# Kernel tuning notes

Measured on AMD Instinct MI355X. Metric: run time of the kernel, lower is better.

The kernel has to match this reference:

```python
import jax, jax.numpy as jnp
import numpy as np

D_MODEL = 1024
NUM_HEADS = 16
D_K = D_MODEL // NUM_HEADS


def setup_inputs() -> dict:
    key = jax.random.key(0)
    ks = jax.random.split(key, 12)
    B, L, D = 1, 4096, D_MODEL
    s = 1.0 / np.sqrt(D)
    return {
        "q": jax.random.normal(ks[0], (B, L, D), jnp.float32),
        "k": jax.random.normal(ks[1], (B, L, D), jnp.float32),
        "v": jax.random.normal(ks[2], (B, L, D), jnp.float32),
        "wq": jax.random.normal(ks[3], (D, D), jnp.float32) * s,
        "bq": jnp.zeros((D,), jnp.float32),
        "wk": jax.random.normal(ks[4], (D, D), jnp.float32) * s,
        "bk": jnp.zeros((D,), jnp.float32),
        "wv": jax.random.normal(ks[5], (D, D), jnp.float32) * s,
        "bv": jnp.zeros((D,), jnp.float32),
        "wo": jax.random.normal(ks[6], (D, D), jnp.float32) * s,
        "bo": jnp.zeros((D,), jnp.float32),
    }


def reference(q, k, v, wq, bq, wk, bk, wv, bv, wo, bo):
    B, L, D = q.shape
    H, dk = NUM_HEADS, D_K
    # linear projections then split heads: [B, L, D] -> [B, H, L, dk]
    def proj(x, w, b):
        return (x @ w.T + b).reshape(B, L, H, dk).transpose(0, 2, 1, 3)
    qh = proj(q, wq, bq)
    kh = proj(k, wk, bk)
    vh = proj(v, wv, bv)
    scores = jnp.einsum("bhqd,bhkd->bhqk", qh, kh) / jnp.sqrt(jnp.float32(dk))
    attn = jax.nn.softmax(scores, axis=-1)  # [B, H, L, L]
    out = jnp.einsum("bhqk,bhkd->bhqd", attn, vh)
    out = out.transpose(0, 2, 1, 3).reshape(B, L, D)
    return out @ wo.T + bo
```

## Files before the change

### kernel.cpp

```cpp
#include <hip/hip_runtime.h>
#include <hip/hip_bf16.h>
#include <stdint.h>


typedef __bf16 bf16_t;
typedef __bf16 bf16x8 __attribute__((ext_vector_type(8)));
typedef __bf16 bf16x4 __attribute__((ext_vector_type(4)));
typedef float f32x4 __attribute__((ext_vector_type(4)));
typedef unsigned short u16x8 __attribute__((ext_vector_type(8)));

#define MFMA_BF16 __builtin_amdgcn_mfma_f32_16x16x32_bf16

__device__ __forceinline__ void async_copy16(const void* g, void* lds) {
  __builtin_amdgcn_global_load_lds(
      (__attribute__((address_space(1))) void*)(uintptr_t)g,
      (__attribute__((address_space(3))) void*)lds, 16, 0, 0);
}

__global__ __launch_bounds__(256) void cast_f32_bf16(
    const float* __restrict__ s0, bf16_t* __restrict__ d0, int n0,
    const float* __restrict__ s1, bf16_t* __restrict__ d1, int n1,
    const float* __restrict__ s2, bf16_t* __restrict__ d2, int n2,
    const float* __restrict__ s3, bf16_t* __restrict__ d3, int n3,
    const float* __restrict__ s4, bf16_t* __restrict__ d4, int n4,
    const float* __restrict__ s5, bf16_t* __restrict__ d5, int n5,
    const float* __restrict__ s6, bf16_t* __restrict__ d6, int n6) {
  const float* s;
  bf16_t* d;
  int n;
  switch (blockIdx.z) {
    case 0: s = s0; d = d0; n = n0; break;
    case 1: s = s1; d = d1; n = n1; break;
    case 2: s = s2; d = d2; n = n2; break;
    case 3: s = s3; d = d3; n = n3; break;
    case 4: s = s4; d = d4; n = n4; break;
    case 5: s = s5; d = d5; n = n5; break;
    default: s = s6; d = d6; n = n6; break;
  }
  const int i = (blockIdx.x * 256 + threadIdx.x) * 8;
  if (i >= n) return;
  float4 a = *(const float4*)(s + i);
  float4 b = *(const float4*)(s + i + 4);
  bf16x8 o;
  o[0] = (bf16_t)a.x; o[1] = (bf16_t)a.y; o[2] = (bf16_t)a.z; o[3] = (bf16_t)a.w;
  o[4] = (bf16_t)b.x; o[5] = (bf16_t)b.y; o[6] = (bf16_t)b.z; o[7] = (bf16_t)b.w;
  *(bf16x8*)(d + i) = o;
}

template <typename CT>
__global__ __launch_bounds__(256) void gemm3_bt(
    const bf16_t* __restrict__ A0, const bf16_t* __restrict__ W0,
    const float* __restrict__ b0, CT* __restrict__ C0,
    const bf16_t* __restrict__ A1, const bf16_t* __restrict__ W1,
    const float* __restrict__ b1, CT* __restrict__ C1,
    const bf16_t* __restrict__ A2, const bf16_t* __restrict__ W2,
    const float* __restrict__ b2, CT* __restrict__ C2,
    int M, int N, int K) {
  const bf16_t *A, *W;
  const float* bias;
  CT* C;
  if (blockIdx.z == 0)      { A = A0; W = W0; bias = b0; C = C0; }
  else if (blockIdx.z == 1) { A = A1; W = W1; bias = b1; C = C1; }
  else                      { A = A2; W = W2; bias = b2; C = C2; }

  __shared__ bf16_t As[128][32];
  __shared__ bf16_t Bs[128][32];

  const int t = threadIdx.x;
  const int w = t >> 6, lane = t & 63;
  const int quad = lane >> 4, l16 = lane & 15;
  const int wr = w >> 1, wc = w & 1;
  const int m0 = blockIdx.x * 128;
  const int n0 = blockIdx.y * 128;
  const int srow = lane >> 2;
  const int scol = (lane & 3) * 8;

  f32x4 acc[4][4] = {};

  for (int k0 = 0; k0 < K; k0 += 32) {
    async_copy16(&A[(size_t)(m0 + (2 * w) * 16 + srow) * K + k0 + scol],
                 (char*)As + (2 * w) * 1024);
    async_copy16(&A[(size_t)(m0 + (2 * w + 1) * 16 + srow) * K + k0 + scol],
                 (char*)As + (2 * w + 1) * 1024);
    async_copy16(&W[(size_t)(n0 + (2 * w) * 16 + srow) * K + k0 + scol],
                 (char*)Bs + (2 * w) * 1024);
    async_copy16(&W[(size_t)(n0 + (2 * w + 1) * 16 + srow) * K + k0 + scol],
                 (char*)Bs + (2 * w + 1) * 1024);
    __syncthreads();

    bf16x8 af[4], bfr[4];
#pragma unroll
    for (int mt = 0; mt < 4; mt++)
      af[mt] = *(const bf16x8*)&As[wr * 64 + mt * 16 + l16][quad * 8];
#pragma unroll
    for (int nt = 0; nt < 4; nt++)
      bfr[nt] = *(const bf16x8*)&Bs[wc * 64 + nt * 16 + l16][quad * 8];
#pragma unroll
    for (int mt = 0; mt < 4; mt++)
#pragma unroll
      for (int nt = 0; nt < 4; nt++)
        acc[mt][nt] = MFMA_BF16(af[mt], bfr[nt], acc[mt][nt], 0, 0, 0);
    __syncthreads();
  }

#pragma unroll
  for (int nt = 0; nt < 4; nt++) {
    const int col = n0 + wc * 64 + nt * 16 + l16;
    const float bb = bias[col];
#pragma unroll
    for (int mt = 0; mt < 4; mt++) {
#pragma unroll
      for (int r = 0; r < 4; r++) {
        const int row = m0 + wr * 64 + mt * 16 + quad * 4 + r;
        C[(size_t)row * N + col] = (CT)(acc[mt][nt][r] + bb);
      }
    }
  }
}

__global__ __launch_bounds__(256) void frag_tile(
    const bf16_t* __restrict__ s0, bf16_t* __restrict__ d0,
    const bf16_t* __restrict__ s1, bf16_t* __restrict__ d1,
    const bf16_t* __restrict__ s2, bf16_t* __restrict__ d2) {
  const bf16_t* src;
  bf16_t* dst;
  const int z = blockIdx.z;
  if (z == 0)      { src = s0; dst = d0; }
  else if (z == 1) { src = s1; dst = d1; }
  else             { src = s2; dst = d2; }

  const int h = blockIdx.y;
  const int l0 = blockIdx.x * 64;
  const int t = threadIdx.x;

  __shared__ ushort Ts[64][72];

#pragma unroll
  for (int p = 0; p < 2; p++) {
    const int r = p * 32 + (t >> 3);
    const int c = (t & 7) * 8;
    float4 v = *(const float4*)(src + (size_t)(l0 + r) * 1024 + h * 64 + c);
    *(float4*)&Ts[r][c] = v;
  }
  __syncthreads();

  if (z < 2) {
    const float qscale = 0.125f * 1.44269504088896340736f;
#pragma unroll
    for (int p = 0; p < 2; p++) {
      const int gi = p * 256 + t;
      const int l16 = gi & 15, quad = (gi >> 4) & 3, kc = (gi >> 6) & 1;
      const int tl = gi >> 7;
      float4 v = *(const float4*)&Ts[tl * 16 + l16][kc * 32 + quad * 8];
      if (z == 0) {
        bf16x8 b = *(bf16x8*)&v;
#pragma unroll
        for (int e = 0; e < 8; e++) b[e] = (bf16_t)((float)b[e] * qscale);
        v = *(float4*)&b;
      }
      *(float4*)(dst + (size_t)(h * 256 + (l0 >> 4) + tl) * 1024 +
                 (size_t)(kc * 64 + quad * 16 + l16) * 8) = v;
    }
  } else {
#pragma unroll
    for (int p = 0; p < 2; p++) {
      const int gi = p * 256 + t;
      const int l16 = gi & 15, quad = (gi >> 4) & 3, kvc = (gi >> 6) & 1;
      const int dkt = gi >> 7;
      u16x8 tmp;
#pragma unroll
      for (int e = 0; e < 8; e++)
        tmp[e] = Ts[kvc * 32 + quad * 4 + (e & 3) + 16 * (e >> 2)]
                   [dkt * 16 + l16];
      *(u16x8*)(dst + (size_t)(h * 256 + (l0 >> 6) * 4 + dkt) * 1024 +
                (size_t)(kvc * 64 + quad * 16 + l16) * 8) = tmp;
    }
  }
}

__global__ __launch_bounds__(512, 4) void flash_attn(
    const bf16_t* __restrict__ Qt, const bf16_t* __restrict__ Kt,
    const bf16_t* __restrict__ Vt, bf16_t* __restrict__ O, int L) {
  const int i = blockIdx.x;
  const int slot = i >> 3;
  const int h = (i & 7) * 2 + (slot >> 5);
  const int qblk = slot & 31;

  const int t = threadIdx.x;
  const int w = t >> 6, lane = t & 63;
  const int quad = lane >> 4, l16 = lane & 15;
  const int g = w >> 2;
  const int ws = w & 3;
  const int tq0 = qblk * 8 + ws * 2;

  __shared__ bf16_t Kst[2][8192];
  __shared__ bf16_t Vst[2][8192];

  const size_t hb = (size_t)h * 256 * 1024;

  union V8 {
    bf16x8 v8;
    bf16x4 v4[2];
  };

  bf16x8 qa[2][2];
#pragma unroll
  for (int qt = 0; qt < 2; qt++)
#pragma unroll
    for (int kc = 0; kc < 2; kc++)
      qa[qt][kc] = *(const bf16x8*)(Qt + hb + (size_t)(tq0 + qt) * 1024 +
                                    kc * 512 + lane * 8);

#define STAGE(mc_, buf_)                                                      \
  {                                                                           \
    const size_t pb_ = hb + (size_t)(mc_) * 8192;                             \
    async_copy16(Kt + pb_ + (size_t)t * 8, (char*)&Kst[buf_][0] + w * 1024);  \
    async_copy16(Kt + pb_ + 4096 + (size_t)t * 8,                             \
                 (char*)&Kst[buf_][0] + 8192 + w * 1024);                     \
    async_copy16(Vt + pb_ + (size_t)t * 8, (char*)&Vst[buf_][0] + w * 1024);  \
    async_copy16(Vt + pb_ + 4096 + (size_t)t * 8,                             \
                 (char*)&Vst[buf_][0] + 8192 + w * 1024);                     \
  }

  STAGE(0, 0);

  f32x4 oT[2][4] = {};
  float ls[2] = {0.f, 0.f};

  const int laneK = lane * 16;

  const int NMC = L / 128;
  for (int mc = 0; mc < NMC; mc++) {
    const int buf = mc & 1;
    __syncthreads();
    if (mc + 1 < NMC) STAGE(mc + 1, buf ^ 1);

    const char* Kc = (const char*)&Kst[buf][0] + g * 8192;
    const char* Vc = (const char*)&Vst[buf][0] + g * 8192;

    f32x4 sT[2][4];
#pragma unroll
    for (int tt = 0; tt < 4; tt++) {
      const bf16x8 k0 = *(const bf16x8*)(Kc + tt * 2048 + laneK);
      const bf16x8 k1 = *(const bf16x8*)(Kc + tt * 2048 + 1024 + laneK);
#pragma unroll
      for (int qt = 0; qt < 2; qt++) {
        f32x4 z = {0.f, 0.f, 0.f, 0.f};
        z = MFMA_BF16(k0, qa[qt][0], z, 0, 0, 0);
        z = MFMA_BF16(k1, qa[qt][1], z, 0, 0, 0);
        sT[qt][tt] = z;
      }
    }

    V8 pb[2][2];
#pragma unroll
    for (int qt = 0; qt < 2; qt++) {
#pragma unroll
      for (int tt = 0; tt < 4; tt++) {
        bf16x4 pk;
        float rs = 0.f;
#pragma unroll
        for (int r = 0; r < 4; r++) {
          const float pv = __builtin_amdgcn_exp2f(sT[qt][tt][r]);
          rs += pv;
          pk[r] = (bf16_t)pv;
        }
        ls[qt] += rs;
        pb[qt][tt >> 1].v4[tt & 1] = pk;
      }
    }

#pragma unroll
    for (int dkt = 0; dkt < 4; dkt++) {
#pragma unroll
      for (int kvc = 0; kvc < 2; kvc++) {
        const bf16x8 vv =
            *(const bf16x8*)(Vc + dkt * 2048 + kvc * 1024 + laneK);
#pragma unroll
        for (int qt = 0; qt < 2; qt++)
          oT[qt][dkt] = MFMA_BF16(vv, pb[qt][kvc].v8, oT[qt][dkt], 0, 0, 0);
      }
    }
  }
#undef STAGE

  __syncthreads();
  float* sc0 = (float*)&Kst[0][0];
  float* sc1 = (float*)&Vst[0][0];
  const int sidx = (ws * 64 + lane) * 20;
  if (g == 1) {
#pragma unroll
    for (int dkt = 0; dkt < 4; dkt++) {
      *(f32x4*)(sc0 + sidx + dkt * 4) = oT[0][dkt];
      *(f32x4*)(sc1 + sidx + dkt * 4) = oT[1][dkt];
    }
    sc0[sidx + 16] = ls[0];
    sc1[sidx + 16] = ls[1];
  }
  __syncthreads();
  if (g == 0) {
#pragma unroll
    for (int dkt = 0; dkt < 4; dkt++) {
      oT[0][dkt] += *(const f32x4*)(sc0 + sidx + dkt * 4);
      oT[1][dkt] += *(const f32x4*)(sc1 + sidx + dkt * 4);
    }
    ls[0] += sc0[sidx + 16];
    ls[1] += sc1[sidx + 16];

#pragma unroll
    for (int qt = 0; qt < 2; qt++) {
      float l = ls[qt];
      l += __shfl_xor(l, 16);
      l += __shfl_xor(l, 32);
      const float inv = 1.0f / l;
      const size_t row = (size_t)(tq0 + qt) * 16 + l16;
#pragma unroll
      for (int dkt = 0; dkt < 4; dkt++)
#pragma unroll
        for (int r = 0; r < 4; r++)
          O[row * 1024 + h * 64 + dkt * 16 + quad * 4 + r] =
              (bf16_t)(oT[qt][dkt][r] * inv);
    }
  }
}

extern "C" void kernel_launch(void* const* d_in, const int* in_sizes, int n_in,
                              void* d_out, int out_size, void* d_ws,
                              size_t ws_size, hipStream_t stream) {
  const float* q  = (const float*)d_in[0];
  const float* k  = (const float*)d_in[1];
  const float* v  = (const float*)d_in[2];
  const float* wq = (const float*)d_in[3];
  const float* bq = (const float*)d_in[4];
  const float* wk = (const float*)d_in[5];
  const float* bk = (const float*)d_in[6];
  const float* wv = (const float*)d_in[7];
  const float* bv = (const float*)d_in[8];
  const float* wo = (const float*)d_in[9];
  const float* bo = (const float*)d_in[10];
  float* out = (float*)d_out;

  const int L = 4096, D = 1024;
  const int nLD = L * D;
  const int nDD = D * D;
  bf16_t* p = (bf16_t*)d_ws;
  bf16_t* qb  = p; p += nLD;
  bf16_t* kb  = p; p += nLD;
  bf16_t* vb  = p; p += nLD;
  bf16_t* wqb = p; p += nDD;
  bf16_t* wkb = p; p += nDD;
  bf16_t* wvb = p; p += nDD;
  bf16_t* wob = p; p += nDD;
  bf16_t* Qp  = p; p += nLD;
  bf16_t* Kp  = p; p += nLD;
  bf16_t* Vp  = p; p += nLD;
  bf16_t* Qt  = p; p += nLD;
  bf16_t* Kt  = p; p += nLD;
  bf16_t* Vt  = p; p += nLD;
  bf16_t* Op  = Qp;

  dim3 blk(256);
  cast_f32_bf16<<<dim3(nLD / (256 * 8), 1, 7), blk, 0, stream>>>(
      q, qb, nLD, k, kb, nLD, v, vb, nLD, wq, wqb, nDD, wk, wkb, nDD,
      wv, wvb, nDD, wo, wob, nDD);
  gemm3_bt<bf16_t><<<dim3(L / 128, D / 128, 3), blk, 0, stream>>>(
      qb, wqb, bq, Qp, kb, wkb, bk, Kp, vb, wvb, bv, Vp, L, D, D);
  frag_tile<<<dim3(L / 64, 16, 3), blk, 0, stream>>>(Qp, Qt, Kp, Kt, Vp, Vt);
  flash_attn<<<dim3((L / 128) * 16), dim3(512), 0, stream>>>(Qt, Kt, Vt, Op, L);
  gemm3_bt<float><<<dim3(L / 128, D / 128, 1), blk, 0, stream>>>(
      Op, wob, bo, out, Op, wob, bo, out, Op, wob, bo, out, L, D, D);
}
```

Before: 264.0 us.

## Fuse fragment retiling into QKV GEMM epilogue and split attention loop barriers

The QKV projection GEMM now writes its outputs directly in the MFMA fragment layout that flash attention consumes, with the Q scale folded in. This removes the separate frag_tile kernel and its extra global read/write pass. The attention loop is also restructured into two phases, QK+softmax and PV, with explicit vmcnt waits, barriers and s_setprio around the MFMA sections, so K and V staging can overlap compute. The cost is scattered, narrow global stores in the GEMM epilogue and more fragile hand-coded wait counts.

```diff
diff --git a/kernel.cpp b/kernel.cpp
--- a/kernel.cpp
+++ b/kernel.cpp
@@ -47,21 +47,21 @@
   *(bf16x8*)(d + i) = o;
 }
 
-template <typename CT>
-__global__ __launch_bounds__(256) void gemm3_bt(
+__global__ __launch_bounds__(256) void gemm_qkv(
     const bf16_t* __restrict__ A0, const bf16_t* __restrict__ W0,
-    const float* __restrict__ b0, CT* __restrict__ C0,
+    const float* __restrict__ b0, bf16_t* __restrict__ D0,
     const bf16_t* __restrict__ A1, const bf16_t* __restrict__ W1,
-    const float* __restrict__ b1, CT* __restrict__ C1,
+    const float* __restrict__ b1, bf16_t* __restrict__ D1,
     const bf16_t* __restrict__ A2, const bf16_t* __restrict__ W2,
-    const float* __restrict__ b2, CT* __restrict__ C2,
+    const float* __restrict__ b2, bf16_t* __restrict__ D2,
     int M, int N, int K) {
   const bf16_t *A, *W;
   const float* bias;
-  CT* C;
-  if (blockIdx.z == 0)      { A = A0; W = W0; bias = b0; C = C0; }
-  else if (blockIdx.z == 1) { A = A1; W = W1; bias = b1; C = C1; }
-  else                      { A = A2; W = W2; bias = b2; C = C2; }
+  bf16_t* D;
+  const int zz = blockIdx.z;
+  if (zz == 0)      { A = A0; W = W0; bias = b0; D = D0; }
+  else if (zz == 1) { A = A1; W = W1; bias = b1; D = D1; }
+  else              { A = A2; W = W2; bias = b2; D = D2; }
 
   __shared__ bf16_t As[128][32];
   __shared__ bf16_t Bs[128][32];
@@ -103,6 +103,95 @@
     __syncthreads();
   }
 
+  if (zz < 2) {
+    const float qs = (zz == 0) ? 0.125f * 1.44269504088896340736f : 1.0f;
+#pragma unroll
+    for (int nt = 0; nt < 4; nt++) {
+      const int col = n0 + wc * 64 + nt * 16 + l16;
+      const int hh = col >> 6, dk = col & 63;
+      const float bb = bias[col];
+      const size_t cbase =
+          (size_t)hh * 256 * 1024 +
+          (size_t)((dk >> 5) * 64 + ((dk >> 3) & 3) * 16) * 8 + (dk & 7);
+#pragma unroll
+      for (int mt = 0; mt < 4; mt++) {
+        const int rowtile = (m0 >> 4) + wr * 4 + mt;
+#pragma unroll
+        for (int r = 0; r < 4; r++) {
+          const int rl = quad * 4 + r;
+          D[cbase + (size_t)rowtile * 1024 + rl * 8] =
+              (bf16_t)((acc[mt][nt][r] + bb) * qs);
+        }
+      }
+    }
+  } else {
+#pragma unroll
+    for (int nt = 0; nt < 4; nt++) {
+      const int col = n0 + wc * 64 + nt * 16 + l16;
+      const int hh = col >> 6, dk = col & 63;
+      const float bb = bias[col];
+#pragma unroll
+      for (int mt = 0; mt < 4; mt++) {
+        const int kvb = m0 + wr * 64 + mt * 16 + quad * 4;
+        const int r50 = kvb & 31;
+        bf16x4 pk;
+#pragma unroll
+        for (int r = 0; r < 4; r++) pk[r] = (bf16_t)(acc[mt][nt][r] + bb);
+        const size_t addr =
+            (size_t)(hh * 256 + (kvb >> 6) * 4 + (dk >> 4)) * 1024 +
+            (size_t)(((kvb >> 5) & 1) * 64 + ((r50 & 15) >> 2) * 16 +
+                     (dk & 15)) * 8 +
+            (((r50 >> 4) & 1) << 2);
+        *(bf16x4*)(D + addr) = pk;
+      }
+    }
+  }
+}
+
+__global__ __launch_bounds__(256) void gemm_out(
+    const bf16_t* __restrict__ A, const bf16_t* __restrict__ W,
+    const float* __restrict__ bias, float* __restrict__ C, int M, int N,
+    int K) {
+  __shared__ bf16_t As[128][32];
+  __shared__ bf16_t Bs[128][32];
+
+  const int t = threadIdx.x;
+  const int w = t >> 6, lane = t & 63;
+  const int quad = lane >> 4, l16 = lane & 15;
+  const int wr = w >> 1, wc = w & 1;
+  const int m0 = blockIdx.x * 128;
+  const int n0 = blockIdx.y * 128;
+  const int srow = lane >> 2;
+  const int scol = (lane & 3) * 8;
+
+  f32x4 acc[4][4] = {};
+
+  for (int k0 = 0; k0 < K; k0 += 32) {
+    async_copy16(&A[(size_t)(m0 + (2 * w) * 16 + srow) * K + k0 + scol],
+                 (char*)As + (2 * w) * 1024);
+    async_copy16(&A[(size_t)(m0 + (2 * w + 1) * 16 + srow) * K + k0 + scol],
+                 (char*)As + (2 * w + 1) * 1024);
+    async_copy16(&W[(size_t)(n0 + (2 * w) * 16 + srow) * K + k0 + scol],
+                 (char*)Bs + (2 * w) * 1024);
+    async_copy16(&W[(size_t)(n0 + (2 * w + 1) * 16 + srow) * K + k0 + scol],
+                 (char*)Bs + (2 * w + 1) * 1024);
+    __syncthreads();
+
+    bf16x8 af[4], bfr[4];
+#pragma unroll
+    for (int mt = 0; mt < 4; mt++)
+      af[mt] = *(const bf16x8*)&As[wr * 64 + mt * 16 + l16][quad * 8];
+#pragma unroll
+    for (int nt = 0; nt < 4; nt++)
+      bfr[nt] = *(const bf16x8*)&Bs[wc * 64 + nt * 16 + l16][quad * 8];
+#pragma unroll
+    for (int mt = 0; mt < 4; mt++)
+#pragma unroll
+      for (int nt = 0; nt < 4; nt++)
+        acc[mt][nt] = MFMA_BF16(af[mt], bfr[nt], acc[mt][nt], 0, 0, 0);
+    __syncthreads();
+  }
+
 #pragma unroll
   for (int nt = 0; nt < 4; nt++) {
     const int col = n0 + wc * 64 + nt * 16 + l16;
@@ -112,68 +201,8 @@
 #pragma unroll
       for (int r = 0; r < 4; r++) {
         const int row = m0 + wr * 64 + mt * 16 + quad * 4 + r;
-        C[(size_t)row * N + col] = (CT)(acc[mt][nt][r] + bb);
+        C[(size_t)row * N + col] = acc[mt][nt][r] + bb;
       }
-    }
-  }
-}
-
-__global__ __launch_bounds__(256) void frag_tile(
-    const bf16_t* __restrict__ s0, bf16_t* __restrict__ d0,
-    const bf16_t* __restrict__ s1, bf16_t* __restrict__ d1,
-    const bf16_t* __restrict__ s2, bf16_t* __restrict__ d2) {
-  const bf16_t* src;
-  bf16_t* dst;
-  const int z = blockIdx.z;
-  if (z == 0)      { src = s0; dst = d0; }
-  else if (z == 1) { src = s1; dst = d1; }
-  else             { src = s2; dst = d2; }
-
-  const int h = blockIdx.y;
-  const int l0 = blockIdx.x * 64;
-  const int t = threadIdx.x;
-
-  __shared__ ushort Ts[64][72];
-
-#pragma unroll
-  for (int p = 0; p < 2; p++) {
-    const int r = p * 32 + (t >> 3);
-    const int c = (t & 7) * 8;
-    float4 v = *(const float4*)(src + (size_t)(l0 + r) * 1024 + h * 64 + c);
-    *(float4*)&Ts[r][c] = v;
-  }
-  __syncthreads();
-
-  if (z < 2) {
-    const float qscale = 0.125f * 1.44269504088896340736f;
-#pragma unroll
-    for (int p = 0; p < 2; p++) {
-      const int gi = p * 256 + t;
-      const int l16 = gi & 15, quad = (gi >> 4) & 3, kc = (gi >> 6) & 1;
-      const int tl = gi >> 7;
-      float4 v = *(const float4*)&Ts[tl * 16 + l16][kc * 32 + quad * 8];
-      if (z == 0) {
-        bf16x8 b = *(bf16x8*)&v;
-#pragma unroll
-        for (int e = 0; e < 8; e++) b[e] = (bf16_t)((float)b[e] * qscale);
-        v = *(float4*)&b;
-      }
-      *(float4*)(dst + (size_t)(h * 256 + (l0 >> 4) + tl) * 1024 +
-                 (size_t)(kc * 64 + quad * 16 + l16) * 8) = v;
-    }
-  } else {
-#pragma unroll
-    for (int p = 0; p < 2; p++) {
-      const int gi = p * 256 + t;
-      const int l16 = gi & 15, quad = (gi >> 4) & 3, kvc = (gi >> 6) & 1;
-      const int dkt = gi >> 7;
-      u16x8 tmp;
-#pragma unroll
-      for (int e = 0; e < 8; e++)
-        tmp[e] = Ts[kvc * 32 + quad * 4 + (e & 3) + 16 * (e >> 2)]
-                   [dkt * 16 + l16];
-      *(u16x8*)(dst + (size_t)(h * 256 + (l0 >> 6) * 4 + dkt) * 1024 +
-                (size_t)(kvc * 64 + quad * 16 + l16) * 8) = tmp;
     }
   }
 }
@@ -222,67 +251,86 @@
                  (char*)&Vst[buf_][0] + 8192 + w * 1024);                     \
   }
 
-  STAGE(0, 0);
-
   f32x4 oT[2][4] = {};
   float ls[2] = {0.f, 0.f};
-
   const int laneK = lane * 16;
+  V8 pb[2][2];
+
+#define PHASE_A(buf_)                                                         \
+  {                                                                           \
+    const char* Kc = (const char*)&Kst[buf_][0] + g * 8192;                   \
+    f32x4 sT[2][4];                                                           \
+    __builtin_amdgcn_s_setprio(1);                                            \
+    _Pragma("unroll") for (int tt = 0; tt < 4; tt++) {                        \
+      const bf16x8 k0 = *(const bf16x8*)(Kc + tt * 2048 + laneK);             \
+      const bf16x8 k1 = *(const bf16x8*)(Kc + tt * 2048 + 1024 + laneK);      \
+      _Pragma("unroll") for (int qt = 0; qt < 2; qt++) {                      \
+        f32x4 z = {0.f, 0.f, 0.f, 0.f};                                       \
+        z = MFMA_BF16(k0, qa[qt][0], z, 0, 0, 0);                             \
+        z = MFMA_BF16(k1, qa[qt][1], z, 0, 0, 0);                             \
+        sT[qt][tt] = z;                                                       \
+      }                                                                       \
+    }                                                                         \
+    __builtin_amdgcn_s_setprio(0);                                            \
+    _Pragma("unroll") for (int qt = 0; qt < 2; qt++) {                        \
+      _Pragma("unroll") for (int tt = 0; tt < 4; tt++) {                      \
+        bf16x4 pk;                                                            \
+        float rs = 0.f;                                                       \
+        _Pragma("unroll") for (int r = 0; r < 4; r++) {                       \
+          const float pv = __builtin_amdgcn_exp2f(sT[qt][tt][r]);             \
+          rs += pv;                                                           \
+          pk[r] = (bf16_t)pv;                                                 \
+        }                                                                     \
+        ls[qt] += rs;                                                         \
+        pb[qt][tt >> 1].v4[tt & 1] = pk;                                      \
+      }                                                                       \
+    }                                                                         \
+  }
+
+#define PHASE_B(buf_)                                                         \
+  {                                                                           \
+    const char* Vc = (const char*)&Vst[buf_][0] + g * 8192;                   \
+    __builtin_amdgcn_s_setprio(1);                                            \
+    _Pragma("unroll") for (int dkt = 0; dkt < 4; dkt++) {                     \
+      _Pragma("unroll") for (int kvc = 0; kvc < 2; kvc++) {                   \
+        const bf16x8 vv =                                                     \
+            *(const bf16x8*)(Vc + dkt * 2048 + kvc * 1024 + laneK);           \
+        _Pragma("unroll") for (int qt = 0; qt < 2; qt++)                      \
+            oT[qt][dkt] = MFMA_BF16(vv, pb[qt][kvc].v8, oT[qt][dkt], 0, 0, 0);\
+      }                                                                       \
+    }                                                                         \
+    __builtin_amdgcn_s_setprio(0);                                            \
+  }
+
+  STAGE(0, 0);
 
   const int NMC = L / 128;
-  for (int mc = 0; mc < NMC; mc++) {
+  for (int mc = 0; mc < NMC - 1; mc++) {
     const int buf = mc & 1;
-    __syncthreads();
-    if (mc + 1 < NMC) STAGE(mc + 1, buf ^ 1);
-
-    const char* Kc = (const char*)&Kst[buf][0] + g * 8192;
-    const char* Vc = (const char*)&Vst[buf][0] + g * 8192;
-
-    f32x4 sT[2][4];
-#pragma unroll
-    for (int tt = 0; tt < 4; tt++) {
-      const bf16x8 k0 = *(const bf16x8*)(Kc + tt * 2048 + laneK);
-      const bf16x8 k1 = *(const bf16x8*)(Kc + tt * 2048 + 1024 + laneK);
-#pragma unroll
-      for (int qt = 0; qt < 2; qt++) {
-        f32x4 z = {0.f, 0.f, 0.f, 0.f};
-        z = MFMA_BF16(k0, qa[qt][0], z, 0, 0, 0);
-        z = MFMA_BF16(k1, qa[qt][1], z, 0, 0, 0);
-        sT[qt][tt] = z;
-      }
-    }
-
-    V8 pb[2][2];
-#pragma unroll
-    for (int qt = 0; qt < 2; qt++) {
-#pragma unroll
-      for (int tt = 0; tt < 4; tt++) {
-        bf16x4 pk;
-        float rs = 0.f;
-#pragma unroll
-        for (int r = 0; r < 4; r++) {
-          const float pv = __builtin_amdgcn_exp2f(sT[qt][tt][r]);
-          rs += pv;
-          pk[r] = (bf16_t)pv;
-        }
-        ls[qt] += rs;
-        pb[qt][tt >> 1].v4[tt & 1] = pk;
-      }
-    }
-
-#pragma unroll
-    for (int dkt = 0; dkt < 4; dkt++) {
-#pragma unroll
-      for (int kvc = 0; kvc < 2; kvc++) {
-        const bf16x8 vv =
-            *(const bf16x8*)(Vc + dkt * 2048 + kvc * 1024 + laneK);
-#pragma unroll
-        for (int qt = 0; qt < 2; qt++)
-          oT[qt][dkt] = MFMA_BF16(vv, pb[qt][kvc].v8, oT[qt][dkt], 0, 0, 0);
-      }
-    }
+    asm volatile("s_waitcnt vmcnt(2)" ::: "memory");
+    __builtin_amdgcn_s_barrier();
+    __builtin_amdgcn_sched_barrier(0);
+    STAGE(mc + 1, buf ^ 1);
+    PHASE_A(buf);
+    asm volatile("s_waitcnt vmcnt(4)" ::: "memory");
+    __builtin_amdgcn_s_barrier();
+    __builtin_amdgcn_sched_barrier(0);
+    PHASE_B(buf);
+  }
+  {
+    const int buf = (NMC - 1) & 1;
+    asm volatile("s_waitcnt vmcnt(2)" ::: "memory");
+    __builtin_amdgcn_s_barrier();
+    __builtin_amdgcn_sched_barrier(0);
+    PHASE_A(buf);
+    asm volatile("s_waitcnt vmcnt(0)" ::: "memory");
+    __builtin_amdgcn_s_barrier();
+    __builtin_amdgcn_sched_barrier(0);
+    PHASE_B(buf);
   }
 #undef STAGE
+#undef PHASE_A
+#undef PHASE_B
 
   __syncthreads();
   float* sc0 = (float*)&Kst[0][0];
@@ -351,22 +399,18 @@
   bf16_t* wkb = p; p += nDD;
   bf16_t* wvb = p; p += nDD;
   bf16_t* wob = p; p += nDD;
-  bf16_t* Qp  = p; p += nLD;
-  bf16_t* Kp  = p; p += nLD;
-  bf16_t* Vp  = p; p += nLD;
+  bf16_t* Op  = p; p += nLD;
   bf16_t* Qt  = p; p += nLD;
   bf16_t* Kt  = p; p += nLD;
   bf16_t* Vt  = p; p += nLD;
-  bf16_t* Op  = Qp;
 
   dim3 blk(256);
   cast_f32_bf16<<<dim3(nLD / (256 * 8), 1, 7), blk, 0, stream>>>(
       q, qb, nLD, k, kb, nLD, v, vb, nLD, wq, wqb, nDD, wk, wkb, nDD,
       wv, wvb, nDD, wo, wob, nDD);
-  gemm3_bt<bf16_t><<<dim3(L / 128, D / 128, 3), blk, 0, stream>>>(
-      qb, wqb, bq, Qp, kb, wkb, bk, Kp, vb, wvb, bv, Vp, L, D, D);
-  frag_tile<<<dim3(L / 64, 16, 3), blk, 0, stream>>>(Qp, Qt, Kp, Kt, Vp, Vt);
+  gemm_qkv<<<dim3(L / 128, D / 128, 3), blk, 0, stream>>>(
+      qb, wqb, bq, Qt, kb, wkb, bk, Kt, vb, wvb, bv, Vt, L, D, D);
   flash_attn<<<dim3((L / 128) * 16), dim3(512), 0, stream>>>(Qt, Kt, Vt, Op, L);
-  gemm3_bt<float><<<dim3(L / 128, D / 128, 1), blk, 0, stream>>>(
-      Op, wob, bo, out, Op, wob, bo, out, Op, wob, bo, out, L, D, D);
-}
+  gemm_out<<<dim3(L / 128, D / 128), blk, 0, stream>>>(Op, wob, bo, out, L, D,
+                                                       D);
+}
```

Result: no change. 264.6 us (+0.2%).
